# Optimization experiments

Measured on AMD Instinct MI355X. Metric: run time of the kernel, lower is better.

## Reference

```python
import jax, jax.numpy as jnp
import numpy as np

LABEL_SMOOTH = 0.1

def setup_inputs() -> dict:
    key = jax.random.key(0)
    k1, k2, k3, k4 = jax.random.split(key, 4)
    B, S, D, V = 2, 2048, 1024, 50257
    targets = jax.random.randint(k1, (B, S), 0, V)              # int labels in [0, V)
    masks = jax.random.randint(k2, (B, S), 0, 2).astype(bool)   # valid-token mask
    outputs = jax.random.normal(k3, (B, S, D), dtype=jnp.float32)
    W = jax.random.normal(k4, (V, D), dtype=jnp.float32) * 0.02  # nn.Linear(d_model, V, bias=False).weight
    return {"targets": targets, "masks": masks, "outputs": outputs, "W": W}

def reference(targets, masks, outputs, W):
    # Faithful to IO.cost: gather masked tokens, project to vocab, label-smoothed NLL.
    # Boolean gather is expressed as mask-weighted means (identical math, jit-friendly).
    V = W.shape[0]
    logits = jnp.einsum('bsd,vd->bsv', outputs, W)        # [B,S,V] huge intermediate
    logp = jax.nn.log_softmax(logits, axis=-1)            # [B,S,V]
    m = masks.astype(logp.dtype)                          # [B,S]
    n_valid = m.sum()
    # F.nll_loss(logits, targets): mean of -logp[target] over valid tokens
    tok_logp = jnp.take_along_axis(logp, targets[..., None], axis=-1)[..., 0]  # [B,S]
    nll = -(m * tok_logp).sum() / n_valid
    # logits.mean(): mean of log-probs over valid tokens x vocab
    mean_logp = (m * logp.sum(axis=-1)).sum() / (n_valid * V)
    return nll * (1.0 - LABEL_SMOOTH) - mean_logp * LABEL_SMOOTH
```

## Files before the change

kernel.cpp:

```cpp
#include <hip/hip_runtime.h>
#include <hip/hip_bf16.h>
#include <stdint.h>

#define T_TOK 4096
#define DIM   1024
#define VOC   50257
#define NBT   400
#define VPAD  (NBT*128)
#define MT    32
#define BM    128
#define BN    128
#define BK    128
#define NKS   8

#define FRAGB  2048
#define PANB   16384

#define WSCALE 64.0f
#define INV_WSCALE 0.015625f

typedef __attribute__((ext_vector_type(8))) int  i32x8;
typedef __attribute__((ext_vector_type(4))) float f32x4;

typedef __attribute__((address_space(3))) uint8_t as3_u8;
typedef __attribute__((address_space(1))) const uint8_t as1_u8;

__device__ __forceinline__ void gload16(const void* g, void* l) {
  __builtin_amdgcn_global_load_lds((as1_u8*)g, (as3_u8*)l, 16, 0, 0);
}

__device__ __forceinline__ uint32_t pk4_fp8(float a, float b, float c, float d) {
  int u = 0;
  u = __builtin_amdgcn_cvt_pk_fp8_f32(a, b, u, false);
  u = __builtin_amdgcn_cvt_pk_fp8_f32(c, d, u, true);
  return (uint32_t)u;
}

__device__ __forceinline__ size_t tiled_off(int row, int k) {
  const int p = row >> 4;
  const int s = k >> 7;
  const int q = (k >> 5) & 3;
  const int h = (k >> 4) & 1;
  const int b = k & 15;
  const int lp = q * 16 + (row & 15);
  return (size_t)(p * 8 + s) * FRAGB + h * 1024 + lp * 16 + b;
}

__global__ void k_scan(const int* __restrict__ masks, const int* __restrict__ targets,
                       int* __restrict__ hdr, int* __restrict__ cidx, int* __restrict__ tgtc,
                       float* __restrict__ Se, float* __restrict__ Sl) {
  __shared__ int cnt[256];
  const int tid = threadIdx.x;
  const int base = tid * 16;
  #pragma unroll
  for (int i = 0; i < 16; i++) { Se[base + i] = 0.f; Sl[base + i] = 0.f; }
  int c = 0;
  #pragma unroll
  for (int i = 0; i < 16; i++) c += (masks[base + i] != 0) ? 1 : 0;
  cnt[tid] = c;
  __syncthreads();
  for (int off = 1; off < 256; off <<= 1) {
    int add = (tid >= off) ? cnt[tid - off] : 0;
    __syncthreads();
    cnt[tid] += add;
    __syncthreads();
  }
  int start = cnt[tid] - c;
  for (int i = 0; i < 16; i++) {
    int t = base + i;
    if (masks[t] != 0) { cidx[start] = t; tgtc[start] = targets[t]; start++; }
  }
  if (tid == 255) hdr[0] = cnt[255];
}

__global__ void k_xconv(const float* __restrict__ X, const int* __restrict__ hdr,
                        const int* __restrict__ cidx, uint8_t* __restrict__ XqT) {
  const int sl = blockIdx.x;
  const int tid = threadIdx.x;
  const int nv = hdr[0];
  uint32_t o = 0;
  if (sl < nv) {
    const float4 v = ((const float4*)(X + (size_t)cidx[sl] * DIM))[tid];
    o = pk4_fp8(v.x, v.y, v.z, v.w);
  }
  *(uint32_t*)&XqT[tiled_off(sl, tid * 4)] = o;
}

__global__ void k_wconv(const float* __restrict__ W, uint8_t* __restrict__ WqT) {
  const size_t stride = (size_t)gridDim.x * blockDim.x;
  const size_t nvec = (size_t)VPAD * DIM / 4;
  const size_t nreal = (size_t)VOC * DIM / 4;
  for (size_t i = (size_t)blockIdx.x * blockDim.x + threadIdx.x; i < nvec; i += stride) {
    uint32_t o = 0;
    if (i < nreal) {
      const float4 v = ((const float4*)W)[i];
      o = pk4_fp8(v.x * WSCALE, v.y * WSCALE, v.z * WSCALE, v.w * WSCALE);
    }
    const size_t e = i * 4;
    *(uint32_t*)&WqT[tiled_off((int)(e >> 10), (int)(e & 1023))] = o;
  }
}

__global__ __launch_bounds__(256) void k_gemm(
    const uint8_t* __restrict__ XqT, const uint8_t* __restrict__ WqT,
    const int* __restrict__ hdr, const int* __restrict__ tgtc,
    float* __restrict__ tlog, float* __restrict__ Se, float* __restrict__ Sl) {
  const int flat = blockIdx.x;
  const int xcd = flat & 7;
  const int sidx = flat >> 3;
  const int mt = sidx & (MT - 1);
  const int nt = (sidx >> 5) * 8 + xcd;

  const int nv = hdr[0];
  const int m0 = mt * BM;
  if (m0 >= nv) return;
  const int n0 = nt * BN;

  __shared__ __align__(16) uint8_t Ash[2][BM * BK];
  __shared__ __align__(16) uint8_t Bsh[2][BN * BK];
  __shared__ float redA[2][BM];
  __shared__ float redB[2][BM];
  __shared__ int tgts[BM];

  const int tid = threadIdx.x;
  const int w    = tid >> 6;
  const int lane = tid & 63;
  const int wy = w >> 1, wx = w & 1;
  const int l15  = lane & 15;
  const int quad = lane >> 4;

  if (tid < BM) tgts[tid] = (m0 + tid < nv) ? tgtc[m0 + tid] : -1;

  const uint8_t* gA = XqT + (size_t)(mt * 8 + 2 * w) * PANB + lane * 16;
  const uint8_t* gB = WqT + (size_t)(nt * 8 + 2 * w) * PANB + lane * 16;
  const int la0 = (2 * w) * FRAGB;
  const int la1 = (2 * w + 1) * FRAGB;

  f32x4 acc[4][4];
  #pragma unroll
  for (int i = 0; i < 4; i++)
    #pragma unroll
    for (int j = 0; j < 4; j++) { f32x4 z = {0.f, 0.f, 0.f, 0.f}; acc[i][j] = z; }

  const int sc1 = 0x7F7F7F7F;

  {
    gload16(gA,               &Ash[0][la0]);
    gload16(gA + 1024,        &Ash[0][la0 + 1024]);
    gload16(gA + PANB,        &Ash[0][la1]);
    gload16(gA + PANB + 1024, &Ash[0][la1 + 1024]);
    gload16(gB,               &Bsh[0][la0]);
    gload16(gB + 1024,        &Bsh[0][la0 + 1024]);
    gload16(gB + PANB,        &Bsh[0][la1]);
    gload16(gB + PANB + 1024, &Bsh[0][la1 + 1024]);
  }

  #pragma unroll
  for (int s = 0; s < NKS; s++) {
    __syncthreads();
    if (s < NKS - 1) {
      const int nb = (s + 1) & 1;
      const size_t so = (size_t)(s + 1) * FRAGB;
      gload16(gA + so,               &Ash[nb][la0]);
      gload16(gA + so + 1024,        &Ash[nb][la0 + 1024]);
      gload16(gA + so + PANB,        &Ash[nb][la1]);
      gload16(gA + so + PANB + 1024, &Ash[nb][la1 + 1024]);
      gload16(gB + so,               &Bsh[nb][la0]);
      gload16(gB + so + 1024,        &Bsh[nb][la0 + 1024]);
      gload16(gB + so + PANB,        &Bsh[nb][la1]);
      gload16(gB + so + PANB + 1024, &Bsh[nb][la1 + 1024]);
    }
    const uint8_t* bufA = Ash[s & 1];
    const uint8_t* bufB = Bsh[s & 1];

    i32x8 a[4], b[4];
    #pragma unroll
    for (int mi = 0; mi < 4; mi++) {
      const int fb = (wy * 4 + mi) * FRAGB + lane * 16;
      const int4 lo = *(const int4*)&bufA[fb];
      const int4 hi = *(const int4*)&bufA[fb + 1024];
      a[mi][0] = lo.x; a[mi][1] = lo.y; a[mi][2] = lo.z; a[mi][3] = lo.w;
      a[mi][4] = hi.x; a[mi][5] = hi.y; a[mi][6] = hi.z; a[mi][7] = hi.w;
    }
    #pragma unroll
    for (int ni = 0; ni < 4; ni++) {
      const int fb = (wx * 4 + ni) * FRAGB + lane * 16;
      const int4 lo = *(const int4*)&bufB[fb];
      const int4 hi = *(const int4*)&bufB[fb + 1024];
      b[ni][0] = lo.x; b[ni][1] = lo.y; b[ni][2] = lo.z; b[ni][3] = lo.w;
      b[ni][4] = hi.x; b[ni][5] = hi.y; b[ni][6] = hi.z; b[ni][7] = hi.w;
    }
    #pragma unroll
    for (int mi = 0; mi < 4; mi++)
      #pragma unroll
      for (int ni = 0; ni < 4; ni++)
        acc[mi][ni] = __builtin_amdgcn_mfma_scale_f32_16x16x128_f8f6f4(
            a[mi], b[ni], acc[mi][ni], 0, 0, 0, sc1, 0, sc1);
  }

  float rse[4][4], rsl[4][4];
  #pragma unroll
  for (int mi = 0; mi < 4; mi++)
    #pragma unroll
    for (int r = 0; r < 4; r++) { rse[mi][r] = 0.f; rsl[mi][r] = 0.f; }
  #pragma unroll
  for (int ni = 0; ni < 4; ni++) {
    const int v = n0 + wx * 64 + ni * 16 + l15;
    if (v < VOC) {
      #pragma unroll
      for (int mi = 0; mi < 4; mi++)
        #pragma unroll
        for (int r = 0; r < 4; r++) {
          const int row = wy * 64 + mi * 16 + quad * 4 + r;
          const float x = acc[mi][ni][r] * INV_WSCALE;
          rse[mi][r] += __expf(x);
          rsl[mi][r] += x;
          if (v == tgts[row]) tlog[m0 + row] = x;
        }
    }
  }
  #pragma unroll
  for (int off = 1; off < 16; off <<= 1)
    #pragma unroll
    for (int mi = 0; mi < 4; mi++)
      #pragma unroll
      for (int r = 0; r < 4; r++) {
        rse[mi][r] += __shfl_xor(rse[mi][r], off, 16);
        rsl[mi][r] += __shfl_xor(rsl[mi][r], off, 16);
      }
  if (l15 == 0) {
    #pragma unroll
    for (int mi = 0; mi < 4; mi++)
      #pragma unroll
      for (int r = 0; r < 4; r++) {
        const int row = wy * 64 + mi * 16 + quad * 4 + r;
        redA[wx][row] = rse[mi][r];
        redB[wx][row] = rsl[mi][r];
      }
  }
  __syncthreads();
  if (tid < BM) {
    const int t = m0 + tid;
    if (t < nv) {
      atomicAdd(&Se[t], redA[0][tid] + redA[1][tid]);
      atomicAdd(&Sl[t], redB[0][tid] + redB[1][tid]);
    }
  }
}

__global__ void k_final(const int* __restrict__ hdr, const float* __restrict__ Se,
                        const float* __restrict__ Sl, const float* __restrict__ tlog,
                        float* __restrict__ out) {
  __shared__ float rn[256], rs[256];
  const int tid = threadIdx.x;
  const int nv = hdr[0];
  float nll = 0.f, slg = 0.f;
  for (int t = tid; t < nv; t += 256) {
    const float lse = logf(Se[t]);
    nll += lse - tlog[t];
    slg += Sl[t] - (float)VOC * lse;
  }
  rn[tid] = nll; rs[tid] = slg;
  __syncthreads();
  for (int off = 128; off > 0; off >>= 1) {
    if (tid < off) { rn[tid] += rn[tid + off]; rs[tid] += rs[tid + off]; }
    __syncthreads();
  }
  if (tid == 0) {
    const float fnv = (float)nv;
    out[0] = 0.9f * (rn[0] / fnv) - 0.1f * (rs[0] / (fnv * (float)VOC));
  }
}

extern "C" void kernel_launch(void* const* d_in, const int* in_sizes, int n_in,
                              void* d_out, int out_size, void* d_ws, size_t ws_size,
                              hipStream_t stream) {
  const int*   targets = (const int*)d_in[0];
  const int*   masks   = (const int*)d_in[1];
  const float* X       = (const float*)d_in[2];
  const float* W       = (const float*)d_in[3];

  uint8_t* ws = (uint8_t*)d_ws;
  size_t off = 0;
  auto alloc = [&](size_t n) { size_t p = off; off += (n + 255) & ~(size_t)255; return p; };
  int*      hdr  = (int*)     (ws + alloc(256));
  int*      cidx = (int*)     (ws + alloc((size_t)T_TOK * 4));
  int*      tgtc = (int*)     (ws + alloc((size_t)T_TOK * 4));
  float*    tlog = (float*)   (ws + alloc((size_t)T_TOK * 4));
  float*    Se   = (float*)   (ws + alloc((size_t)T_TOK * 4));
  float*    Sl   = (float*)   (ws + alloc((size_t)T_TOK * 4));
  uint8_t*  XqT  = (uint8_t*) (ws + alloc((size_t)T_TOK * DIM));
  uint8_t*  WqT  = (uint8_t*) (ws + alloc((size_t)VPAD * DIM));

  k_scan<<<dim3(1), dim3(256), 0, stream>>>(masks, targets, hdr, cidx, tgtc, Se, Sl);
  k_xconv<<<dim3(T_TOK), dim3(256), 0, stream>>>(X, hdr, cidx, XqT);
  k_wconv<<<dim3(8192), dim3(256), 0, stream>>>(W, WqT);
  k_gemm<<<dim3(MT * NBT), dim3(256), 0, stream>>>(XqT, WqT, hdr, tgtc, tlog, Se, Sl);
  k_final<<<dim3(1), dim3(256), 0, stream>>>(hdr, Se, Sl, tlog, (float*)d_out);
}
```

Baseline: 680.2 us.

## Load fp8 MFMA fragments directly from global with per-lane 32-byte layout

Changes the pre-packed fp8 fragment layout so each lane owns 32 contiguous bytes. The GEMM now loads operands straight into registers with software double buffering instead of staging through LDS with barriers. Tiles become 64 tokens by 256 vocab entries, with each wave computing its own 64x64 block. The conversion kernels now do one fragment lane per thread, using coalesced 32-byte stores in place of scattered 4-byte writes. The change trades LDS reuse across waves for more global and L2 traffic, and it drops the per-step syncs.

After: 577.3 us. 1.18x faster.

```diff
diff --git a/kernel.cpp b/kernel.cpp
--- a/kernel.cpp
+++ b/kernel.cpp
@@ -5,11 +5,7 @@
 #define T_TOK 4096
 #define DIM   1024
 #define VOC   50257
-#define NBT   400
-#define VPAD  (NBT*128)
-#define MT    32
-#define BM    128
-#define BN    128
+#define VPAD  51200
 #define BK    128
 #define NKS   8
 
@@ -21,13 +17,6 @@
 
 typedef __attribute__((ext_vector_type(8))) int  i32x8;
 typedef __attribute__((ext_vector_type(4))) float f32x4;
-
-typedef __attribute__((address_space(3))) uint8_t as3_u8;
-typedef __attribute__((address_space(1))) const uint8_t as1_u8;
-
-__device__ __forceinline__ void gload16(const void* g, void* l) {
-  __builtin_amdgcn_global_load_lds((as1_u8*)g, (as3_u8*)l, 16, 0, 0);
-}
 
 __device__ __forceinline__ uint32_t pk4_fp8(float a, float b, float c, float d) {
   int u = 0;
@@ -36,14 +25,13 @@
   return (uint32_t)u;
 }
 
-__device__ __forceinline__ size_t tiled_off(int row, int k) {
-  const int p = row >> 4;
-  const int s = k >> 7;
-  const int q = (k >> 5) & 3;
-  const int h = (k >> 4) & 1;
-  const int b = k & 15;
-  const int lp = q * 16 + (row & 15);
-  return (size_t)(p * 8 + s) * FRAGB + h * 1024 + lp * 16 + b;
+__device__ __forceinline__ i32x8 ld32(const uint8_t* p) {
+  const int4 lo = *(const int4*)p;
+  const int4 hi = *(const int4*)(p + 16);
+  i32x8 r;
+  r[0] = lo.x; r[1] = lo.y; r[2] = lo.z; r[3] = lo.w;
+  r[4] = hi.x; r[5] = hi.y; r[6] = hi.z; r[7] = hi.w;
+  return r;
 }
 
 __global__ void k_scan(const int* __restrict__ masks, const int* __restrict__ targets,
@@ -75,30 +63,46 @@
 
 __global__ void k_xconv(const float* __restrict__ X, const int* __restrict__ hdr,
                         const int* __restrict__ cidx, uint8_t* __restrict__ XqT) {
-  const int sl = blockIdx.x;
-  const int tid = threadIdx.x;
+  const int c = blockIdx.x * 256 + threadIdx.x;
+  const int f = c >> 6;
+  const int l = c & 63;
+  const int p = f >> 3, s = f & 7;
+  const int sl = p * 16 + (l & 15);
+  const int kb = s * 128 + (l >> 4) * 32;
   const int nv = hdr[0];
-  uint32_t o = 0;
+  uint32_t o[8] = {0, 0, 0, 0, 0, 0, 0, 0};
   if (sl < nv) {
-    const float4 v = ((const float4*)(X + (size_t)cidx[sl] * DIM))[tid];
-    o = pk4_fp8(v.x, v.y, v.z, v.w);
-  }
-  *(uint32_t*)&XqT[tiled_off(sl, tid * 4)] = o;
+    const float* src = X + (size_t)cidx[sl] * DIM + kb;
+    #pragma unroll
+    for (int j = 0; j < 8; j++) {
+      const float4 v = ((const float4*)src)[j];
+      o[j] = pk4_fp8(v.x, v.y, v.z, v.w);
+    }
+  }
+  int4* dst = (int4*)(XqT + (size_t)c * 32);
+  dst[0] = make_int4(o[0], o[1], o[2], o[3]);
+  dst[1] = make_int4(o[4], o[5], o[6], o[7]);
 }
 
 __global__ void k_wconv(const float* __restrict__ W, uint8_t* __restrict__ WqT) {
-  const size_t stride = (size_t)gridDim.x * blockDim.x;
-  const size_t nvec = (size_t)VPAD * DIM / 4;
-  const size_t nreal = (size_t)VOC * DIM / 4;
-  for (size_t i = (size_t)blockIdx.x * blockDim.x + threadIdx.x; i < nvec; i += stride) {
-    uint32_t o = 0;
-    if (i < nreal) {
-      const float4 v = ((const float4*)W)[i];
-      o = pk4_fp8(v.x * WSCALE, v.y * WSCALE, v.z * WSCALE, v.w * WSCALE);
-    }
-    const size_t e = i * 4;
-    *(uint32_t*)&WqT[tiled_off((int)(e >> 10), (int)(e & 1023))] = o;
-  }
+  const int c = blockIdx.x * 256 + threadIdx.x;
+  const int f = c >> 6;
+  const int l = c & 63;
+  const int p = f >> 3, s = f & 7;
+  const int row = p * 16 + (l & 15);
+  const int kb = s * 128 + (l >> 4) * 32;
+  uint32_t o[8] = {0, 0, 0, 0, 0, 0, 0, 0};
+  if (row < VOC) {
+    const float* src = W + (size_t)row * DIM + kb;
+    #pragma unroll
+    for (int j = 0; j < 8; j++) {
+      const float4 v = ((const float4*)src)[j];
+      o[j] = pk4_fp8(v.x * WSCALE, v.y * WSCALE, v.z * WSCALE, v.w * WSCALE);
+    }
+  }
+  int4* dst = (int4*)(WqT + (size_t)c * 32);
+  dst[0] = make_int4(o[0], o[1], o[2], o[3]);
+  dst[1] = make_int4(o[4], o[5], o[6], o[7]);
 }
 
 __global__ __launch_bounds__(256) void k_gemm(
@@ -107,34 +111,28 @@
     float* __restrict__ tlog, float* __restrict__ Se, float* __restrict__ Sl) {
   const int flat = blockIdx.x;
   const int xcd = flat & 7;
-  const int sidx = flat >> 3;
-  const int mt = sidx & (MT - 1);
-  const int nt = (sidx >> 5) * 8 + xcd;
+  const int u = flat >> 3;
+  const int ms = u & 63;
+  const int ng = (u >> 6) * 8 + xcd;
 
   const int nv = hdr[0];
-  const int m0 = mt * BM;
+  const int m0 = ms * 64;
   if (m0 >= nv) return;
-  const int n0 = nt * BN;
-
-  __shared__ __align__(16) uint8_t Ash[2][BM * BK];
-  __shared__ __align__(16) uint8_t Bsh[2][BN * BK];
-  __shared__ float redA[2][BM];
-  __shared__ float redB[2][BM];
-  __shared__ int tgts[BM];
 
   const int tid = threadIdx.x;
   const int w    = tid >> 6;
   const int lane = tid & 63;
-  const int wy = w >> 1, wx = w & 1;
+  const int quad = lane >> 4;
   const int l15  = lane & 15;
-  const int quad = lane >> 4;
-
-  if (tid < BM) tgts[tid] = (m0 + tid < nv) ? tgtc[m0 + tid] : -1;
-
-  const uint8_t* gA = XqT + (size_t)(mt * 8 + 2 * w) * PANB + lane * 16;
-  const uint8_t* gB = WqT + (size_t)(nt * 8 + 2 * w) * PANB + lane * 16;
-  const int la0 = (2 * w) * FRAGB;
-  const int la1 = (2 * w + 1) * FRAGB;
+  const int n0w  = (ng * 4 + w) * 64;
+
+  const uint8_t* pA[4];
+  const uint8_t* pB[4];
+  #pragma unroll
+  for (int i = 0; i < 4; i++) {
+    pA[i] = XqT + (size_t)(ms * 4 + i) * PANB + lane * 32;
+    pB[i] = WqT + (size_t)((n0w >> 4) + i) * PANB + lane * 32;
+  }
 
   f32x4 acc[4][4];
   #pragma unroll
@@ -144,60 +142,48 @@
 
   const int sc1 = 0x7F7F7F7F;
 
-  {
-    gload16(gA,               &Ash[0][la0]);
-    gload16(gA + 1024,        &Ash[0][la0 + 1024]);
-    gload16(gA + PANB,        &Ash[0][la1]);
-    gload16(gA + PANB + 1024, &Ash[0][la1 + 1024]);
-    gload16(gB,               &Bsh[0][la0]);
-    gload16(gB + 1024,        &Bsh[0][la0 + 1024]);
-    gload16(gB + PANB,        &Bsh[0][la1]);
-    gload16(gB + PANB + 1024, &Bsh[0][la1 + 1024]);
-  }
-
-  #pragma unroll
-  for (int s = 0; s < NKS; s++) {
-    __syncthreads();
-    if (s < NKS - 1) {
-      const int nb = (s + 1) & 1;
-      const size_t so = (size_t)(s + 1) * FRAGB;
-      gload16(gA + so,               &Ash[nb][la0]);
-      gload16(gA + so + 1024,        &Ash[nb][la0 + 1024]);
-      gload16(gA + so + PANB,        &Ash[nb][la1]);
-      gload16(gA + so + PANB + 1024, &Ash[nb][la1 + 1024]);
-      gload16(gB + so,               &Bsh[nb][la0]);
-      gload16(gB + so + 1024,        &Bsh[nb][la0 + 1024]);
-      gload16(gB + so + PANB,        &Bsh[nb][la1]);
-      gload16(gB + so + PANB + 1024, &Bsh[nb][la1 + 1024]);
-    }
-    const uint8_t* bufA = Ash[s & 1];
-    const uint8_t* bufB = Bsh[s & 1];
-
-    i32x8 a[4], b[4];
-    #pragma unroll
-    for (int mi = 0; mi < 4; mi++) {
-      const int fb = (wy * 4 + mi) * FRAGB + lane * 16;
-      const int4 lo = *(const int4*)&bufA[fb];
-      const int4 hi = *(const int4*)&bufA[fb + 1024];
-      a[mi][0] = lo.x; a[mi][1] = lo.y; a[mi][2] = lo.z; a[mi][3] = lo.w;
-      a[mi][4] = hi.x; a[mi][5] = hi.y; a[mi][6] = hi.z; a[mi][7] = hi.w;
-    }
-    #pragma unroll
-    for (int ni = 0; ni < 4; ni++) {
-      const int fb = (wx * 4 + ni) * FRAGB + lane * 16;
-      const int4 lo = *(const int4*)&bufB[fb];
-      const int4 hi = *(const int4*)&bufB[fb + 1024];
-      b[ni][0] = lo.x; b[ni][1] = lo.y; b[ni][2] = lo.z; b[ni][3] = lo.w;
-      b[ni][4] = hi.x; b[ni][5] = hi.y; b[ni][6] = hi.z; b[ni][7] = hi.w;
+  i32x8 a0[4], b0[4], a1[4], b1[4];
+  #pragma unroll
+  for (int i = 0; i < 4; i++) { a0[i] = ld32(pA[i]); b0[i] = ld32(pB[i]); }
+
+  #pragma unroll
+  for (int s = 0; s < NKS; s += 2) {
+    if (s + 1 < NKS) {
+      #pragma unroll
+      for (int i = 0; i < 4; i++) {
+        a1[i] = ld32(pA[i] + (s + 1) * FRAGB);
+        b1[i] = ld32(pB[i] + (s + 1) * FRAGB);
+      }
     }
     #pragma unroll
     for (int mi = 0; mi < 4; mi++)
       #pragma unroll
       for (int ni = 0; ni < 4; ni++)
         acc[mi][ni] = __builtin_amdgcn_mfma_scale_f32_16x16x128_f8f6f4(
-            a[mi], b[ni], acc[mi][ni], 0, 0, 0, sc1, 0, sc1);
-  }
-
+            a0[mi], b0[ni], acc[mi][ni], 0, 0, 0, sc1, 0, sc1);
+    if (s + 2 < NKS) {
+      #pragma unroll
+      for (int i = 0; i < 4; i++) {
+        a0[i] = ld32(pA[i] + (s + 2) * FRAGB);
+        b0[i] = ld32(pB[i] + (s + 2) * FRAGB);
+      }
+    }
+    if (s + 1 < NKS) {
+      #pragma unroll
+      for (int mi = 0; mi < 4; mi++)
+        #pragma unroll
+        for (int ni = 0; ni < 4; ni++)
+          acc[mi][ni] = __builtin_amdgcn_mfma_scale_f32_16x16x128_f8f6f4(
+              a1[mi], b1[ni], acc[mi][ni], 0, 0, 0, sc1, 0, sc1);
+    }
+  }
+
+  int tg[4][4];
+  #pragma unroll
+  for (int mi = 0; mi < 4; mi++) {
+    const int4 t4 = *(const int4*)&tgtc[m0 + mi * 16 + quad * 4];
+    tg[mi][0] = t4.x; tg[mi][1] = t4.y; tg[mi][2] = t4.z; tg[mi][3] = t4.w;
+  }
   float rse[4][4], rsl[4][4];
   #pragma unroll
   for (int mi = 0; mi < 4; mi++)
@@ -205,17 +191,16 @@
     for (int r = 0; r < 4; r++) { rse[mi][r] = 0.f; rsl[mi][r] = 0.f; }
   #pragma unroll
   for (int ni = 0; ni < 4; ni++) {
-    const int v = n0 + wx * 64 + ni * 16 + l15;
+    const int v = n0w + ni * 16 + l15;
     if (v < VOC) {
       #pragma unroll
       for (int mi = 0; mi < 4; mi++)
         #pragma unroll
         for (int r = 0; r < 4; r++) {
-          const int row = wy * 64 + mi * 16 + quad * 4 + r;
           const float x = acc[mi][ni][r] * INV_WSCALE;
           rse[mi][r] += __expf(x);
           rsl[mi][r] += x;
-          if (v == tgts[row]) tlog[m0 + row] = x;
+          if (v == tg[mi][r]) tlog[m0 + mi * 16 + quad * 4 + r] = x;
         }
     }
   }
@@ -228,22 +213,24 @@
         rse[mi][r] += __shfl_xor(rse[mi][r], off, 16);
         rsl[mi][r] += __shfl_xor(rsl[mi][r], off, 16);
       }
+
+  __shared__ float seP[4][64], slP[4][64];
   if (l15 == 0) {
     #pragma unroll
     for (int mi = 0; mi < 4; mi++)
       #pragma unroll
       for (int r = 0; r < 4; r++) {
-        const int row = wy * 64 + mi * 16 + quad * 4 + r;
-        redA[wx][row] = rse[mi][r];
-        redB[wx][row] = rsl[mi][r];
+        const int row = mi * 16 + quad * 4 + r;
+        seP[w][row] = rse[mi][r];
+        slP[w][row] = rsl[mi][r];
       }
   }
   __syncthreads();
-  if (tid < BM) {
+  if (tid < 64) {
     const int t = m0 + tid;
     if (t < nv) {
-      atomicAdd(&Se[t], redA[0][tid] + redA[1][tid]);
-      atomicAdd(&Sl[t], redB[0][tid] + redB[1][tid]);
+      atomicAdd(&Se[t], seP[0][tid] + seP[1][tid] + seP[2][tid] + seP[3][tid]);
+      atomicAdd(&Sl[t], slP[0][tid] + slP[1][tid] + slP[2][tid] + slP[3][tid]);
     }
   }
 }
@@ -293,8 +280,8 @@
   uint8_t*  WqT  = (uint8_t*) (ws + alloc((size_t)VPAD * DIM));
 
   k_scan<<<dim3(1), dim3(256), 0, stream>>>(masks, targets, hdr, cidx, tgtc, Se, Sl);
-  k_xconv<<<dim3(T_TOK), dim3(256), 0, stream>>>(X, hdr, cidx, XqT);
-  k_wconv<<<dim3(8192), dim3(256), 0, stream>>>(W, WqT);
-  k_gemm<<<dim3(MT * NBT), dim3(256), 0, stream>>>(XqT, WqT, hdr, tgtc, tlog, Se, Sl);
+  k_xconv<<<dim3(T_TOK * DIM / 32 / 256), dim3(256), 0, stream>>>(X, hdr, cidx, XqT);
+  k_wconv<<<dim3(VPAD * DIM / 32 / 256), dim3(256), 0, stream>>>(W, WqT);
+  k_gemm<<<dim3(64 * 200), dim3(256), 0, stream>>>(XqT, WqT, hdr, tgtc, tlog, Se, Sl);
   k_final<<<dim3(1), dim3(256), 0, stream>>>(hdr, Se, Sl, tlog, (float*)d_out);
 }
```
